# Optimization experiments

Measured on AMD Instinct MI355X. Metric: run time of the kernel, lower is better.

The kernel has to match this reference:

```python
import jax, jax.numpy as jnp
import numpy as np
from jax import lax


def setup_inputs() -> dict:
    key = jax.random.key(0)
    ks = jax.random.split(key, 20)
    B, D, T = 1024, 256, 128
    H, O = 256, 64
    f32 = jnp.float32
    rn = lambda k, shape, sc: jax.random.normal(k, shape, f32) * sc
    ru = lambda k, shape: jax.random.uniform(k, shape, f32)
    return {
        "x": jax.random.normal(ks[0], (B, D, T), f32),
        "W_in": rn(ks[1], (H, D), 1.0 / np.sqrt(D)),
        "b_in": rn(ks[2], (H,), 0.02),
        "beta1": ru(ks[3], (H,)),
        "thr1": ru(ks[4], (H,)),
        "W_h": rn(ks[5], (H, H), 1.0 / np.sqrt(H)),
        "b_h": rn(ks[6], (H,), 0.02),
        "beta2": ru(ks[7], (H,)),
        "thr2": ru(ks[8], (H,)),
        "W_h1": rn(ks[9], (H, H), 1.0 / np.sqrt(H)),
        "b_h1": rn(ks[10], (H,), 0.02),
        "W_f": rn(ks[11], (O, H), 1.0 / np.sqrt(H)),
        "b_f": rn(ks[12], (O,), 0.02),
        "beta_f": ru(ks[13], (O,)),
        "W_a": rn(ks[14], (O, H), 1.0 / np.sqrt(H)),
        "b_a": rn(ks[15], (O,), 0.02),
        "beta_a": ru(ks[16], (O,)),
    }


def _spike(u):
    # heaviside(u > 0); surrogate grad only matters in backward
    return (u > 0).astype(u.dtype)


def reference(x, W_in, b_in, beta1, thr1, W_h, b_h, beta2, thr2,
              W_h1, b_h1, W_f, b_f, beta_f, W_a, b_a, beta_a):
    B = x.shape[0]
    H0, H1, H2 = W_in.shape[0], W_h.shape[0], W_h1.shape[0]
    O = W_f.shape[0]
    dt = x.dtype
    # snntorch clamps learnable beta to [0, 1] in the state update
    b1c = jnp.clip(beta1, 0.0, 1.0)
    b2c = jnp.clip(beta2, 0.0, 1.0)
    bfc = jnp.clip(beta_f, 0.0, 1.0)
    bac = jnp.clip(beta_a, 0.0, 1.0)
    xT = jnp.transpose(x, (2, 0, 1))  # [T, B, D]

    def lif(mem, cur, bc, thr):
        # snntorch Leaky, reset_mechanism='subtract': reset from PREVIOUS mem (detached)
        reset = lax.stop_gradient(_spike(mem - thr))
        mem = bc * mem + cur - reset * thr
        spk = _spike(mem - thr)
        return spk, mem

    def step(carry, xt):
        m1, m2, m3, mf, ma = carry
        cur1 = xt @ W_in.T + b_in
        s1, m1 = lif(m1, cur1, b1c, thr1)
        cur2 = s1 @ W_h.T + b_h
        s2, m2 = lif(m2, cur2, b2c, thr2)
        # source bug preserved: third layer reuses lif_hidden (beta2, thr2)
        cur3 = s2 @ W_h1.T + b_h1
        s3, m3 = lif(m3, cur3, b2c, thr2)
        # output LI neurons: reset_mechanism='none'
        mf = bfc * mf + (s3 @ W_f.T + b_f)
        ma = bac * ma + (s3 @ W_a.T + b_a)
        return (m1, m2, m3, mf, ma), None

    z = lambda n: jnp.zeros((B, n), dt)
    init = (z(H0), z(H1), z(H2), z(O), z(O))
    (m1, m2, m3, mf, ma), _ = lax.scan(step, init, xT)
    return jax.nn.sigmoid(mf), jax.nn.sigmoid(ma)
```

## Files before the change

### kernel.cpp

```cpp
#include <hip/hip_runtime.h>
#include <math.h>
#include <stdint.h>


namespace {

constexpr int Bsz = 1024;
constexpr int Dd  = 256;
constexpr int Tt  = 128;
constexpr int Hh  = 256;
constexpr int Oo  = 64;

__global__ void pack_t(const float* __restrict__ W, float* __restrict__ Wt,
                       int R, int C) {
    int idx = blockIdx.x * 256 + threadIdx.x;
    if (idx >= (C + 1) * R) return;
    int c = idx / R, r = idx - c * R;
    Wt[idx] = (c < C) ? W[(size_t)r * C + c] : 0.f;
}

__global__ void pack_o(const float* __restrict__ Wf, const float* __restrict__ Wa,
                       float* __restrict__ WtO) {
    int idx = blockIdx.x * 256 + threadIdx.x;
    if (idx >= 257 * 128) return;
    int k = idx >> 7, o = idx & 127;
    float v = 0.f;
    if (k < 256) v = (o < 64) ? Wf[(size_t)o * 256 + k] : Wa[(size_t)(o - 64) * 256 + k];
    WtO[idx] = v;
}

__device__ __forceinline__ float clamp01(float v) { return fminf(fmaxf(v, 0.f), 1.f); }

__device__ __forceinline__ bool lif_step(float& m, float cur, float B, float Th) {
    const float r = (__fsub_rn(m, Th) > 0.f) ? Th : 0.f;
    m = __fsub_rn(__fadd_rn(__fmul_rn(B, m), cur), r);
    return __fsub_rn(m, Th) > 0.f;
}

__device__ __forceinline__ void make_masks(int nib, int lane, uint64_t* M) {
    #pragma unroll
    for (int q = 0; q < 4; ++q) {
        const int v   = __shfl(nib, 16 * q + (lane >> 2), 64);
        const int bit = (v >> (lane & 3)) & 1;
        M[q] = __ballot(bit != 0);
    }
}

__device__ __forceinline__ int compact(int nib, int lane, const uint64_t* M,
                                       uint16_t* lst) {
    const int p0 = (int)__popcll(M[0]);
    const int p1 = (int)__popcll(M[1]);
    const int p2 = (int)__popcll(M[2]);
    const int p3 = (int)__popcll(M[3]);
    const int q  = lane >> 4;
    const int base = ((q >= 1) ? p0 : 0) + ((q >= 2) ? p1 : 0) + ((q >= 3) ? p2 : 0);
    const uint64_t mq = (q & 2) ? ((q & 1) ? M[3] : M[2])
                                : ((q & 1) ? M[1] : M[0]);
    const int posb = (lane & 15) << 2;
    const int r0 = base + (int)__popcll(mq & ((1ull << posb) - 1ull));
    const int s1 = nib & 1;
    const int s2 = s1 + ((nib >> 1) & 1);
    const int s3 = s2 + ((nib >> 2) & 1);
    const int nb = lane << 2;
    if (nib & 1) lst[r0]      = (uint16_t)nb;
    if (nib & 2) lst[r0 + s1] = (uint16_t)(nb + 1);
    if (nib & 4) lst[r0 + s2] = (uint16_t)(nb + 2);
    if (nib & 8) lst[r0 + s3] = (uint16_t)(nb + 3);
    const int n    = p0 + p1 + p2 + p3;
    const int npad = (n + 7) & ~7;
    if (lane < npad - n) lst[n + lane] = (uint16_t)Hh;
    return npad;
}


__device__ __forceinline__ void issue8h(const char* __restrict__ tab,
                                        uint4 I, int offB, float4* w) {
    const int k[8] = {(int)(I.x & 0xffff), (int)(I.x >> 16),
                      (int)(I.y & 0xffff), (int)(I.y >> 16),
                      (int)(I.z & 0xffff), (int)(I.z >> 16),
                      (int)(I.w & 0xffff), (int)(I.w >> 16)};
    #pragma unroll
    for (int i = 0; i < 8; ++i)
        w[i] = *(const float4*)(tab + (k[i] << 10) + offB);
}

__device__ __forceinline__ void cons8h(float4& c, const float4* w) {
    #pragma unroll
    for (int i = 0; i < 8; ++i) {
        c.x = __fadd_rn(c.x, w[i].x);
        c.y = __fadd_rn(c.y, w[i].y);
        c.z = __fadd_rn(c.z, w[i].z);
        c.w = __fadd_rn(c.w, w[i].w);
    }
}

__device__ __forceinline__ float4 sum_h(const uint16_t* lst, int nbat,
                                        const float* __restrict__ tab, int offB) {
    float4 c = {0.f, 0.f, 0.f, 0.f};
    if (nbat == 0) return c;
    const char* tb = (const char*)tab;
    float4 A[8], B[8], C[8];
    issue8h(tb, *(const uint4*)(lst), offB, A);
    if (nbat == 1) { cons8h(c, A); return c; }
    issue8h(tb, *(const uint4*)(lst + 8), offB, B);
    if (nbat == 2) { cons8h(c, A); cons8h(c, B); return c; }
    issue8h(tb, *(const uint4*)(lst + 16), offB, C);
    __builtin_amdgcn_sched_barrier(0);
    int i = 3;
    for (; i + 2 < nbat; i += 3) {
        cons8h(c, A); issue8h(tb, *(const uint4*)(lst + 8 * i), offB, A);
        __builtin_amdgcn_sched_barrier(0);
        cons8h(c, B); issue8h(tb, *(const uint4*)(lst + 8 * (i + 1)), offB, B);
        __builtin_amdgcn_sched_barrier(0);
        cons8h(c, C); issue8h(tb, *(const uint4*)(lst + 8 * (i + 2)), offB, C);
        __builtin_amdgcn_sched_barrier(0);
    }
    const int r = nbat - i;
    if (r == 0) {
        cons8h(c, A); cons8h(c, B); cons8h(c, C);
    } else if (r == 1) {
        cons8h(c, A); issue8h(tb, *(const uint4*)(lst + 8 * i), offB, A);
        cons8h(c, B); cons8h(c, C); cons8h(c, A);
    } else {
        cons8h(c, A); issue8h(tb, *(const uint4*)(lst + 8 * i), offB, A);
        cons8h(c, B); issue8h(tb, *(const uint4*)(lst + 8 * (i + 1)), offB, B);
        cons8h(c, C); cons8h(c, A); cons8h(c, B);
    }
    return c;
}


__device__ __forceinline__ float2 sum_o_lds(const uint16_t* lst, int nbat,
                                            const float* tab, int offB) {
    float2 c = {0.f, 0.f};
    const char* tb = (const char*)tab;
    for (int i = 0; i < nbat; ++i) {
        const uint4 I = *(const uint4*)(lst + 8 * i);
        float2 w[8];
        w[0] = *(const float2*)(tb + ((I.x & 0xffffu) << 9) + offB);
        w[1] = *(const float2*)(tb + ((I.x >> 16)    << 9) + offB);
        w[2] = *(const float2*)(tb + ((I.y & 0xffffu) << 9) + offB);
        w[3] = *(const float2*)(tb + ((I.y >> 16)    << 9) + offB);
        w[4] = *(const float2*)(tb + ((I.z & 0xffffu) << 9) + offB);
        w[5] = *(const float2*)(tb + ((I.z >> 16)    << 9) + offB);
        w[6] = *(const float2*)(tb + ((I.w & 0xffffu) << 9) + offB);
        w[7] = *(const float2*)(tb + ((I.w >> 16)    << 9) + offB);
        #pragma unroll
        for (int j = 0; j < 8; ++j) {
            c.x = __fadd_rn(c.x, w[j].x);
            c.y = __fadd_rn(c.y, w[j].y);
        }
    }
    return c;
}

__global__ __launch_bounds__(256, 1) void snn_rec(
    const float* __restrict__ cur1,
    const float* __restrict__ Wt_h, const float* __restrict__ Wt_h1,
    const float* __restrict__ WtO,
    const float* __restrict__ beta1, const float* __restrict__ thr1,
    const float* __restrict__ b_h,  const float* __restrict__ beta2, const float* __restrict__ thr2,
    const float* __restrict__ b_h1,
    const float* __restrict__ b_f,  const float* __restrict__ beta_f,
    const float* __restrict__ b_a,  const float* __restrict__ beta_a,
    float* __restrict__ m1s, float* __restrict__ m2s, float* __restrict__ m3s,
    float* __restrict__ mos, float* __restrict__ out,
    int TC, int first)
{
    __shared__ __attribute__((aligned(16))) float ldsO[257 * 128];
    __shared__ __attribute__((aligned(16))) uint16_t lists[4][272];

    const int tid  = threadIdx.x;
    const int lane = tid & 63;
    const int b    = blockIdx.x * 4 + (tid >> 6);
    uint16_t* lst  = lists[tid >> 6];
    const int off4 = lane * 4;
    const int off2 = lane * 2;
    const int offBh = lane * 16;
    const int offBo = lane * 8;

    {
        const float4* s4 = (const float4*)WtO;
        float4* d4 = (float4*)ldsO;
        for (int v = tid; v < (257 * 128) / 4; v += 256) d4[v] = s4[v];
    }
    __syncthreads();

    const float4 B1v  = *(const float4*)(beta1 + off4);
    const float4 Th1v = *(const float4*)(thr1  + off4);
    const float4 bhv  = *(const float4*)(b_h   + off4);
    const float4 B2v  = *(const float4*)(beta2 + off4);
    const float4 Th2v = *(const float4*)(thr2  + off4);
    const float4 bh1v = *(const float4*)(b_h1  + off4);
    const float4 B1c  = {clamp01(B1v.x), clamp01(B1v.y), clamp01(B1v.z), clamp01(B1v.w)};
    const float4 B2c  = {clamp01(B2v.x), clamp01(B2v.y), clamp01(B2v.z), clamp01(B2v.w)};

    const int oo = off2 & 63;
    const float* bop = (lane < 32) ? b_f    : b_a;
    const float* Bop = (lane < 32) ? beta_f : beta_a;
    const float bo0 = bop[oo], bo1 = bop[oo + 1];
    const float Bo0 = clamp01(Bop[oo]), Bo1 = clamp01(Bop[oo + 1]);

    float4 m1, m2, m3;
    float mo0, mo1;
    if (first) {
        m1 = m2 = m3 = make_float4(0.f, 0.f, 0.f, 0.f);
        mo0 = mo1 = 0.f;
    } else {
        m1 = *(const float4*)(m1s + (size_t)b * Hh + off4);
        m2 = *(const float4*)(m2s + (size_t)b * Hh + off4);
        m3 = *(const float4*)(m3s + (size_t)b * Hh + off4);
        const float2 mo = *(const float2*)(mos + (size_t)b * 128 + off2);
        mo0 = mo.x; mo1 = mo.y;
    }

    const float* __restrict__ curb = cur1 + (size_t)b * TC * Hh + off4;
    float4 cur = *(const float4*)(curb);
    uint64_t M[4];

    for (int t = 0; t < TC; ++t) {
        int nib = 0;
        nib |= (int)lif_step(m1.x, cur.x, B1c.x, Th1v.x);
        nib |= (int)lif_step(m1.y, cur.y, B1c.y, Th1v.y) << 1;
        nib |= (int)lif_step(m1.z, cur.z, B1c.z, Th1v.z) << 2;
        nib |= (int)lif_step(m1.w, cur.w, B1c.w, Th1v.w) << 3;
        make_masks(nib, lane, M);
        int npad = compact(nib, lane, M, lst);
        if (t + 1 < TC) cur = *(const float4*)(curb + (size_t)(t + 1) * Hh);

        float4 s = sum_h(lst, npad >> 3, Wt_h, offBh);
        nib  = (int)lif_step(m2.x, __fadd_rn(s.x, bhv.x), B2c.x, Th2v.x);
        nib |= (int)lif_step(m2.y, __fadd_rn(s.y, bhv.y), B2c.y, Th2v.y) << 1;
        nib |= (int)lif_step(m2.z, __fadd_rn(s.z, bhv.z), B2c.z, Th2v.z) << 2;
        nib |= (int)lif_step(m2.w, __fadd_rn(s.w, bhv.w), B2c.w, Th2v.w) << 3;
        make_masks(nib, lane, M);
        npad = compact(nib, lane, M, lst);

        s = sum_h(lst, npad >> 3, Wt_h1, offBh);
        nib  = (int)lif_step(m3.x, __fadd_rn(s.x, bh1v.x), B2c.x, Th2v.x);
        nib |= (int)lif_step(m3.y, __fadd_rn(s.y, bh1v.y), B2c.y, Th2v.y) << 1;
        nib |= (int)lif_step(m3.z, __fadd_rn(s.z, bh1v.z), B2c.z, Th2v.z) << 2;
        nib |= (int)lif_step(m3.w, __fadd_rn(s.w, bh1v.w), B2c.w, Th2v.w) << 3;
        make_masks(nib, lane, M);
        npad = compact(nib, lane, M, lst);

        const float2 os = sum_o_lds(lst, npad >> 3, ldsO, offBo);
        mo0 = __fadd_rn(__fmul_rn(Bo0, mo0), __fadd_rn(os.x, bo0));
        mo1 = __fadd_rn(__fmul_rn(Bo1, mo1), __fadd_rn(os.y, bo1));
    }

    *(float4*)(m1s + (size_t)b * Hh + off4) = m1;
    *(float4*)(m2s + (size_t)b * Hh + off4) = m2;
    *(float4*)(m3s + (size_t)b * Hh + off4) = m3;
    *(float2*)(mos + (size_t)b * 128 + off2) = make_float2(mo0, mo1);

    float* dst = out + ((lane < 32) ? 0 : (size_t)Bsz * Oo) + (size_t)b * Oo + oo;
    const float o0 = (float)(1.0 / (1.0 + exp(-(double)mo0)));
    const float o1 = (float)(1.0 / (1.0 + exp(-(double)mo1)));
    *(float2*)dst = make_float2(o0, o1);
}

template<int TT>
__global__ __launch_bounds__(256) void gemm_l1_r8(
    const float* __restrict__ x, const float* __restrict__ Wt_in,
    const float* __restrict__ b_in, float* __restrict__ cur1,
    int tg_base, int TCloc)
{
    __shared__ float xs[Dd][TT];
    const int tid = threadIdx.x;
    const int b   = blockIdx.x;
    const int ty  = blockIdx.y;
    const int tg0 = tg_base + ty * TT;
    const float* xb = x + (size_t)b * Dd * Tt + tg0;
    constexpr int T4 = TT / 4;
    for (int v = tid; v < Dd * T4; v += 256) {
        const int d = v / T4, j4 = v - d * T4;
        *(float4*)&xs[d][j4 * 4] = *(const float4*)(xb + (size_t)d * Tt + j4 * 4);
    }
    __syncthreads();
    constexpr int TS = TT / 4;
    const int hq = tid & 63;
    const int tq = tid >> 6;
    float c0[TS], c1[TS], c2[TS], c3[TS];
    #pragma unroll
    for (int j = 0; j < TS; ++j) { c0[j] = 0.f; c1[j] = 0.f; c2[j] = 0.f; c3[j] = 0.f; }
    const float* wp = Wt_in + hq * 4;
    #pragma unroll 4
    for (int d = 0; d < Dd; ++d) {
        const float4 w = *(const float4*)(wp + (size_t)d * Hh);
        #pragma unroll
        for (int j = 0; j < TS; ++j) {
            const float xv = xs[d][tq * TS + j];
            c0[j] = fmaf(w.x, xv, c0[j]);
            c1[j] = fmaf(w.y, xv, c1[j]);
            c2[j] = fmaf(w.z, xv, c2[j]);
            c3[j] = fmaf(w.w, xv, c3[j]);
        }
    }
    const float4 bb = *(const float4*)(b_in + hq * 4);
    float* cb = cur1 + ((size_t)b * TCloc + ty * TT + tq * TS) * Hh + hq * 4;
    #pragma unroll
    for (int j = 0; j < TS; ++j) {
        float4 o;
        o.x = __fadd_rn(c0[j], bb.x);
        o.y = __fadd_rn(c1[j], bb.y);
        o.z = __fadd_rn(c2[j], bb.z);
        o.w = __fadd_rn(c3[j], bb.w);
        *(float4*)(cb + (size_t)j * Hh) = o;
    }
}

template<int TT>
__global__ __launch_bounds__(256) void gemm_l1_lds(
    const float* __restrict__ x, const float* __restrict__ Wt_in,
    const float* __restrict__ b_in, float* __restrict__ cur1,
    int tg_base, int TCloc)
{
    __shared__ float xs[Dd][TT];
    const int h   = threadIdx.x;
    const int b   = blockIdx.x;
    const int ty  = blockIdx.y;
    const int tg0 = tg_base + ty * TT;
    const float* xb = x + (size_t)b * Dd * Tt + tg0;
    constexpr int T4 = TT / 4;
    for (int v = threadIdx.x; v < Dd * T4; v += 256) {
        const int d = v / T4, j4 = v - d * T4;
        *(float4*)&xs[d][j4 * 4] = *(const float4*)(xb + (size_t)d * Tt + j4 * 4);
    }
    __syncthreads();
    float c[TT];
    #pragma unroll
    for (int j = 0; j < TT; ++j) c[j] = 0.f;
    for (int d = 0; d < Dd; ++d) {
        const float w = Wt_in[d * Hh + h];
        #pragma unroll
        for (int j = 0; j < TT; ++j) c[j] = fmaf(w, xs[d][j], c[j]);
    }
    const float bb = b_in[h];
    float* cb = cur1 + ((size_t)b * TCloc + ty * TT) * Hh;
    #pragma unroll
    for (int j = 0; j < TT; ++j) cb[j * Hh + h] = __fadd_rn(c[j], bb);
}

template<int TT>
__global__ __launch_bounds__(256) void gemm_l1_simple(
    const float* __restrict__ x, const float* __restrict__ Wt_in,
    const float* __restrict__ b_in, float* __restrict__ cur1, int tg0)
{
    const int h = threadIdx.x;
    const int b = blockIdx.x;
    float c[TT];
    #pragma unroll
    for (int j = 0; j < TT; ++j) c[j] = 0.f;
    const float* xb = x + (size_t)b * Dd * Tt + tg0;
    for (int d = 0; d < Dd; ++d) {
        const float w = Wt_in[d * Hh + h];
        const float* xp = xb + (size_t)d * Tt;
        #pragma unroll
        for (int j = 0; j < TT; ++j) c[j] = fmaf(w, xp[j], c[j]);
    }
    const float bb = b_in[h];
    float* cb = cur1 + (size_t)b * TT * Hh;
    #pragma unroll
    for (int j = 0; j < TT; ++j) cb[j * Hh + h] = __fadd_rn(c[j], bb);
}

}

extern "C" void kernel_launch(void* const* d_in, const int* in_sizes, int n_in,
                              void* d_out, int out_size, void* d_ws, size_t ws_size,
                              hipStream_t stream) {
    const float* x      = (const float*)d_in[0];
    const float* W_in   = (const float*)d_in[1];
    const float* b_in   = (const float*)d_in[2];
    const float* beta1  = (const float*)d_in[3];
    const float* thr1   = (const float*)d_in[4];
    const float* W_h    = (const float*)d_in[5];
    const float* b_h    = (const float*)d_in[6];
    const float* beta2  = (const float*)d_in[7];
    const float* thr2   = (const float*)d_in[8];
    const float* W_h1   = (const float*)d_in[9];
    const float* b_h1   = (const float*)d_in[10];
    const float* W_f    = (const float*)d_in[11];
    const float* b_f    = (const float*)d_in[12];
    const float* beta_f = (const float*)d_in[13];
    const float* W_a    = (const float*)d_in[14];
    const float* b_a    = (const float*)d_in[15];
    const float* beta_a = (const float*)d_in[16];
    float* out = (float*)d_out;

    float* ws = (float*)d_ws;
    size_t off = 0;
    auto alloc = [&](size_t n) { float* p = ws + off; off += n; return p; };
    float* Wt_in = alloc(257 * 256);
    float* Wt_h  = alloc(257 * 256);
    float* Wt_h1 = alloc(257 * 256);
    float* WtO   = alloc(257 * 128);
    float* m1s   = alloc((size_t)Bsz * Hh);
    float* m2s   = alloc((size_t)Bsz * Hh);
    float* m3s   = alloc((size_t)Bsz * Hh);
    float* mos   = alloc((size_t)Bsz * 128);
    const size_t fixed = off;

    int TC = 1;
    const int cands[8] = {128, 64, 32, 16, 8, 4, 2, 1};
    for (int i = 0; i < 8; ++i) {
        if ((fixed + (size_t)cands[i] * Bsz * Hh) * sizeof(float) <= ws_size) { TC = cands[i]; break; }
    }
    float* cur1 = alloc((size_t)TC * Bsz * Hh);

    pack_t<<<257, 256, 0, stream>>>(W_in, Wt_in, 256, 256);
    pack_t<<<257, 256, 0, stream>>>(W_h,  Wt_h,  256, 256);
    pack_t<<<257, 256, 0, stream>>>(W_h1, Wt_h1, 256, 256);
    pack_o<<<129, 256, 0, stream>>>(W_f, W_a, WtO);

    const int nch = Tt / TC;
    for (int c = 0; c < nch; ++c) {
        const int tg = c * TC;
        if (TC >= 32)
            gemm_l1_r8<32><<<dim3(Bsz, TC / 32), 256, 0, stream>>>(x, Wt_in, b_in, cur1, tg, TC);
        else if (TC == 16)
            gemm_l1_lds<16><<<dim3(Bsz, 1), 256, 0, stream>>>(x, Wt_in, b_in, cur1, tg, TC);
        else if (TC == 8)
            gemm_l1_lds<8><<<dim3(Bsz, 1), 256, 0, stream>>>(x, Wt_in, b_in, cur1, tg, TC);
        else if (TC == 4)
            gemm_l1_simple<4><<<Bsz, 256, 0, stream>>>(x, Wt_in, b_in, cur1, tg);
        else if (TC == 2)
            gemm_l1_simple<2><<<Bsz, 256, 0, stream>>>(x, Wt_in, b_in, cur1, tg);
        else
            gemm_l1_simple<1><<<Bsz, 256, 0, stream>>>(x, Wt_in, b_in, cur1, tg);

        snn_rec<<<Bsz / 4, 256, 0, stream>>>(
            cur1, Wt_h, Wt_h1, WtO,
            beta1, thr1, b_h, beta2, thr2, b_h1,
            b_f, beta_f, b_a, beta_a,
            m1s, m2s, m3s, mos, out, TC, (c == 0) ? 1 : 0);
    }
}
```

Measured before the change: 1.129 ms.

## Share one spike-union weight gather across four batch rows per block

Restructures the recurrent kernel so each wave owns 64 hidden units across the block's four batch rows, instead of each wave owning one batch row across all hidden units. Spike masks are published to shared memory with ballots, and the union of active inputs across the four rows is compacted into a list. Each list entry carries a 4-bit row mask, so one weight load feeds four accumulators. This cuts global weight gathers when rows share spikes, but adds three block-wide barriers per timestep and does wasted adds where the rows' spikes do not overlap. Separately, the input GEMM now prefetches the next weight row a loop iteration ahead.

Measured after the change: 2.483 ms. 2.2x slower.

```diff
diff --git a/kernel.cpp b/kernel.cpp
--- a/kernel.cpp
+++ b/kernel.cpp
@@ -37,17 +37,50 @@
     return __fsub_rn(m, Th) > 0.f;
 }
 
-__device__ __forceinline__ void make_masks(int nib, int lane, uint64_t* M) {
-    #pragma unroll
-    for (int q = 0; q < 4; ++q) {
-        const int v   = __shfl(nib, 16 * q + (lane >> 2), 64);
-        const int bit = (v >> (lane & 3)) & 1;
-        M[q] = __ballot(bit != 0);
-    }
-}
-
-__device__ __forceinline__ int compact(int nib, int lane, const uint64_t* M,
-                                       uint16_t* lst) {
+__device__ __forceinline__ int compact_u(int lane, const uint64_t (*mb)[4],
+                                         uint16_t* lst) {
+    const uint64_t m00 = mb[0][0], m10 = mb[1][0], m20 = mb[2][0], m30 = mb[3][0];
+    const uint64_t m01 = mb[0][1], m11 = mb[1][1], m21 = mb[2][1], m31 = mb[3][1];
+    const uint64_t m02 = mb[0][2], m12 = mb[1][2], m22 = mb[2][2], m32 = mb[3][2];
+    const uint64_t m03 = mb[0][3], m13 = mb[1][3], m23 = mb[2][3], m33 = mb[3][3];
+    const uint64_t U0 = m00 | m10 | m20 | m30;
+    const uint64_t U1 = m01 | m11 | m21 | m31;
+    const uint64_t U2 = m02 | m12 | m22 | m32;
+    const uint64_t U3 = m03 | m13 | m23 | m33;
+    const int p0 = (int)__popcll(U0);
+    const int p1 = (int)__popcll(U1);
+    const int p2 = (int)__popcll(U2);
+    const int p3 = (int)__popcll(U3);
+    const int q  = lane >> 4;
+    const uint64_t Uq = (q & 2) ? ((q & 1) ? U3 : U2) : ((q & 1) ? U1 : U0);
+    const uint64_t r0q = (q & 2) ? ((q & 1) ? m03 : m02) : ((q & 1) ? m01 : m00);
+    const uint64_t r1q = (q & 2) ? ((q & 1) ? m13 : m12) : ((q & 1) ? m11 : m10);
+    const uint64_t r2q = (q & 2) ? ((q & 1) ? m23 : m22) : ((q & 1) ? m21 : m20);
+    const uint64_t r3q = (q & 2) ? ((q & 1) ? m33 : m32) : ((q & 1) ? m31 : m30);
+    const int posb = (lane & 15) << 2;
+    const int nib  = (int)((Uq >> posb) & 0xFull);
+    const int base = ((q >= 1) ? p0 : 0) + ((q >= 2) ? p1 : 0) + ((q >= 3) ? p2 : 0);
+    const int r0   = base + (int)__popcll(Uq & ((1ull << posb) - 1ull));
+    const int s1 = nib & 1;
+    const int s2 = s1 + ((nib >> 1) & 1);
+    const int s3 = s2 + ((nib >> 2) & 1);
+    const int nb = lane << 2;
+    #define RM_AT(pos) ( (int)((r0q >> (pos)) & 1)        | ((int)((r1q >> (pos)) & 1) << 1) \
+                       | ((int)((r2q >> (pos)) & 1) << 2) | ((int)((r3q >> (pos)) & 1) << 3) )
+    if (nib & 1) lst[r0]      = (uint16_t)( nb      | (RM_AT(posb    ) << 12));
+    if (nib & 2) lst[r0 + s1] = (uint16_t)((nb + 1) | (RM_AT(posb + 1) << 12));
+    if (nib & 4) lst[r0 + s2] = (uint16_t)((nb + 2) | (RM_AT(posb + 2) << 12));
+    if (nib & 8) lst[r0 + s3] = (uint16_t)((nb + 3) | (RM_AT(posb + 3) << 12));
+    #undef RM_AT
+    const int n    = p0 + p1 + p2 + p3;
+    const int npad = (n + 7) & ~7;
+    if (lane < npad - n) lst[n + lane] = (uint16_t)Hh;
+    return npad;
+}
+
+__device__ __forceinline__ int compact_row(int lane, const uint64_t* M,
+                                           uint16_t* lst) {
+    const int nib = (int)((M[lane >> 4] >> ((lane & 15) << 2)) & 0xFull);
     const int p0 = (int)__popcll(M[0]);
     const int p1 = (int)__popcll(M[1]);
     const int p2 = (int)__popcll(M[2]);
@@ -73,60 +106,71 @@
 }
 
 
-__device__ __forceinline__ void issue8h(const char* __restrict__ tab,
-                                        uint4 I, int offB, float4* w) {
-    const int k[8] = {(int)(I.x & 0xffff), (int)(I.x >> 16),
-                      (int)(I.y & 0xffff), (int)(I.y >> 16),
-                      (int)(I.z & 0xffff), (int)(I.z >> 16),
-                      (int)(I.w & 0xffff), (int)(I.w >> 16)};
+__device__ __forceinline__ void issue8u(const char* __restrict__ tab,
+                                        uint4 I, int offW, float* w) {
+    const int k[8] = {(int)(I.x & 0xFFFu), (int)((I.x >> 16) & 0xFFFu),
+                      (int)(I.y & 0xFFFu), (int)((I.y >> 16) & 0xFFFu),
+                      (int)(I.z & 0xFFFu), (int)((I.z >> 16) & 0xFFFu),
+                      (int)(I.w & 0xFFFu), (int)((I.w >> 16) & 0xFFFu)};
     #pragma unroll
     for (int i = 0; i < 8; ++i)
-        w[i] = *(const float4*)(tab + (k[i] << 10) + offB);
-}
-
-__device__ __forceinline__ void cons8h(float4& c, const float4* w) {
+        w[i] = *(const float*)(tab + (k[i] << 10) + offW);
+}
+
+__device__ __forceinline__ void cons8u(float* acc, const float* w, uint4 I) {
+    const int rm[8] = {(int)((I.x >> 12) & 0xFu), (int)((I.x >> 28) & 0xFu),
+                       (int)((I.y >> 12) & 0xFu), (int)((I.y >> 28) & 0xFu),
+                       (int)((I.z >> 12) & 0xFu), (int)((I.z >> 28) & 0xFu),
+                       (int)((I.w >> 12) & 0xFu), (int)((I.w >> 28) & 0xFu)};
     #pragma unroll
     for (int i = 0; i < 8; ++i) {
-        c.x = __fadd_rn(c.x, w[i].x);
-        c.y = __fadd_rn(c.y, w[i].y);
-        c.z = __fadd_rn(c.z, w[i].z);
-        c.w = __fadd_rn(c.w, w[i].w);
-    }
-}
-
-__device__ __forceinline__ float4 sum_h(const uint16_t* lst, int nbat,
-                                        const float* __restrict__ tab, int offB) {
-    float4 c = {0.f, 0.f, 0.f, 0.f};
-    if (nbat == 0) return c;
+        acc[0] = __fadd_rn(acc[0], (rm[i] & 1) ? w[i] : 0.0f);
+        acc[1] = __fadd_rn(acc[1], (rm[i] & 2) ? w[i] : 0.0f);
+        acc[2] = __fadd_rn(acc[2], (rm[i] & 4) ? w[i] : 0.0f);
+        acc[3] = __fadd_rn(acc[3], (rm[i] & 8) ? w[i] : 0.0f);
+    }
+}
+
+__device__ __forceinline__ void sum_hu(const uint16_t* lst, int nbat,
+                                       const float* __restrict__ tab, int offW,
+                                       float* acc) {
+    acc[0] = 0.f; acc[1] = 0.f; acc[2] = 0.f; acc[3] = 0.f;
+    if (nbat == 0) return;
     const char* tb = (const char*)tab;
-    float4 A[8], B[8], C[8];
-    issue8h(tb, *(const uint4*)(lst), offB, A);
-    if (nbat == 1) { cons8h(c, A); return c; }
-    issue8h(tb, *(const uint4*)(lst + 8), offB, B);
-    if (nbat == 2) { cons8h(c, A); cons8h(c, B); return c; }
-    issue8h(tb, *(const uint4*)(lst + 16), offB, C);
+    uint4 IA, IB, IC;
+    float WA[8], WB[8], WC[8];
+    IA = *(const uint4*)(lst);      issue8u(tb, IA, offW, WA);
+    if (nbat == 1) { cons8u(acc, WA, IA); return; }
+    IB = *(const uint4*)(lst + 8);  issue8u(tb, IB, offW, WB);
+    if (nbat == 2) { cons8u(acc, WA, IA); cons8u(acc, WB, IB); return; }
+    IC = *(const uint4*)(lst + 16); issue8u(tb, IC, offW, WC);
     __builtin_amdgcn_sched_barrier(0);
     int i = 3;
     for (; i + 2 < nbat; i += 3) {
-        cons8h(c, A); issue8h(tb, *(const uint4*)(lst + 8 * i), offB, A);
+        cons8u(acc, WA, IA);
+        IA = *(const uint4*)(lst + 8 * i);       issue8u(tb, IA, offW, WA);
         __builtin_amdgcn_sched_barrier(0);
-        cons8h(c, B); issue8h(tb, *(const uint4*)(lst + 8 * (i + 1)), offB, B);
+        cons8u(acc, WB, IB);
+        IB = *(const uint4*)(lst + 8 * (i + 1)); issue8u(tb, IB, offW, WB);
         __builtin_amdgcn_sched_barrier(0);
-        cons8h(c, C); issue8h(tb, *(const uint4*)(lst + 8 * (i + 2)), offB, C);
+        cons8u(acc, WC, IC);
+        IC = *(const uint4*)(lst + 8 * (i + 2)); issue8u(tb, IC, offW, WC);
         __builtin_amdgcn_sched_barrier(0);
     }
     const int r = nbat - i;
     if (r == 0) {
-        cons8h(c, A); cons8h(c, B); cons8h(c, C);
+        cons8u(acc, WA, IA); cons8u(acc, WB, IB); cons8u(acc, WC, IC);
     } else if (r == 1) {
-        cons8h(c, A); issue8h(tb, *(const uint4*)(lst + 8 * i), offB, A);
-        cons8h(c, B); cons8h(c, C); cons8h(c, A);
+        cons8u(acc, WA, IA);
+        IA = *(const uint4*)(lst + 8 * i); issue8u(tb, IA, offW, WA);
+        cons8u(acc, WB, IB); cons8u(acc, WC, IC); cons8u(acc, WA, IA);
     } else {
-        cons8h(c, A); issue8h(tb, *(const uint4*)(lst + 8 * i), offB, A);
-        cons8h(c, B); issue8h(tb, *(const uint4*)(lst + 8 * (i + 1)), offB, B);
-        cons8h(c, C); cons8h(c, A); cons8h(c, B);
-    }
-    return c;
+        cons8u(acc, WA, IA);
+        IA = *(const uint4*)(lst + 8 * i);       issue8u(tb, IA, offW, WA);
+        cons8u(acc, WB, IB);
+        IB = *(const uint4*)(lst + 8 * (i + 1)); issue8u(tb, IB, offW, WB);
+        cons8u(acc, WC, IC); cons8u(acc, WA, IA); cons8u(acc, WB, IB);
+    }
 }
 
 
@@ -169,14 +213,17 @@
 {
     __shared__ __attribute__((aligned(16))) float ldsO[257 * 128];
     __shared__ __attribute__((aligned(16))) uint16_t lists[4][272];
+    __shared__ __attribute__((aligned(16))) uint64_t mbuf[2][3][4][4];
 
     const int tid  = threadIdx.x;
     const int lane = tid & 63;
-    const int b    = blockIdx.x * 4 + (tid >> 6);
-    uint16_t* lst  = lists[tid >> 6];
-    const int off4 = lane * 4;
+    const int wq   = tid >> 6;
+    const int b0   = blockIdx.x * 4;
+    const int brow = b0 + wq;
+    uint16_t* lst  = lists[wq];
+    const int hq   = wq * 64 + lane;
+    const int offW = hq * 4;
     const int off2 = lane * 2;
-    const int offBh = lane * 16;
     const int offBo = lane * 8;
 
     {
@@ -186,14 +233,12 @@
     }
     __syncthreads();
 
-    const float4 B1v  = *(const float4*)(beta1 + off4);
-    const float4 Th1v = *(const float4*)(thr1  + off4);
-    const float4 bhv  = *(const float4*)(b_h   + off4);
-    const float4 B2v  = *(const float4*)(beta2 + off4);
-    const float4 Th2v = *(const float4*)(thr2  + off4);
-    const float4 bh1v = *(const float4*)(b_h1  + off4);
-    const float4 B1c  = {clamp01(B1v.x), clamp01(B1v.y), clamp01(B1v.z), clamp01(B1v.w)};
-    const float4 B2c  = {clamp01(B2v.x), clamp01(B2v.y), clamp01(B2v.z), clamp01(B2v.w)};
+    const float B1s  = clamp01(beta1[hq]);
+    const float Th1s = thr1[hq];
+    const float bhs  = b_h[hq];
+    const float B2s  = clamp01(beta2[hq]);
+    const float Th2s = thr2[hq];
+    const float bh1s = b_h1[hq];
 
     const int oo = off2 & 63;
     const float* bop = (lane < 32) ? b_f    : b_a;
@@ -201,60 +246,91 @@
     const float bo0 = bop[oo], bo1 = bop[oo + 1];
     const float Bo0 = clamp01(Bop[oo]), Bo1 = clamp01(Bop[oo + 1]);
 
-    float4 m1, m2, m3;
+    float m1a[4], m2a[4], m3a[4];
     float mo0, mo1;
     if (first) {
-        m1 = m2 = m3 = make_float4(0.f, 0.f, 0.f, 0.f);
+        #pragma unroll
+        for (int r = 0; r < 4; ++r) { m1a[r] = 0.f; m2a[r] = 0.f; m3a[r] = 0.f; }
         mo0 = mo1 = 0.f;
     } else {
-        m1 = *(const float4*)(m1s + (size_t)b * Hh + off4);
-        m2 = *(const float4*)(m2s + (size_t)b * Hh + off4);
-        m3 = *(const float4*)(m3s + (size_t)b * Hh + off4);
-        const float2 mo = *(const float2*)(mos + (size_t)b * 128 + off2);
+        #pragma unroll
+        for (int r = 0; r < 4; ++r) {
+            m1a[r] = m1s[(size_t)(b0 + r) * Hh + hq];
+            m2a[r] = m2s[(size_t)(b0 + r) * Hh + hq];
+            m3a[r] = m3s[(size_t)(b0 + r) * Hh + hq];
+        }
+        const float2 mo = *(const float2*)(mos + (size_t)brow * 128 + off2);
         mo0 = mo.x; mo1 = mo.y;
     }
 
-    const float* __restrict__ curb = cur1 + (size_t)b * TC * Hh + off4;
-    float4 cur = *(const float4*)(curb);
-    uint64_t M[4];
+    const float* __restrict__ curb0 = cur1 + ((size_t)(b0 + 0) * TC) * Hh + hq;
+    const float* __restrict__ curb1 = cur1 + ((size_t)(b0 + 1) * TC) * Hh + hq;
+    const float* __restrict__ curb2 = cur1 + ((size_t)(b0 + 2) * TC) * Hh + hq;
+    const float* __restrict__ curb3 = cur1 + ((size_t)(b0 + 3) * TC) * Hh + hq;
+    float cur0 = curb0[0], cur1v = curb1[0], cur2v = curb2[0], cur3v = curb3[0];
+
+    float acc[4];
 
     for (int t = 0; t < TC; ++t) {
-        int nib = 0;
-        nib |= (int)lif_step(m1.x, cur.x, B1c.x, Th1v.x);
-        nib |= (int)lif_step(m1.y, cur.y, B1c.y, Th1v.y) << 1;
-        nib |= (int)lif_step(m1.z, cur.z, B1c.z, Th1v.z) << 2;
-        nib |= (int)lif_step(m1.w, cur.w, B1c.w, Th1v.w) << 3;
-        make_masks(nib, lane, M);
-        int npad = compact(nib, lane, M, lst);
-        if (t + 1 < TC) cur = *(const float4*)(curb + (size_t)(t + 1) * Hh);
-
-        float4 s = sum_h(lst, npad >> 3, Wt_h, offBh);
-        nib  = (int)lif_step(m2.x, __fadd_rn(s.x, bhv.x), B2c.x, Th2v.x);
-        nib |= (int)lif_step(m2.y, __fadd_rn(s.y, bhv.y), B2c.y, Th2v.y) << 1;
-        nib |= (int)lif_step(m2.z, __fadd_rn(s.z, bhv.z), B2c.z, Th2v.z) << 2;
-        nib |= (int)lif_step(m2.w, __fadd_rn(s.w, bhv.w), B2c.w, Th2v.w) << 3;
-        make_masks(nib, lane, M);
-        npad = compact(nib, lane, M, lst);
-
-        s = sum_h(lst, npad >> 3, Wt_h1, offBh);
-        nib  = (int)lif_step(m3.x, __fadd_rn(s.x, bh1v.x), B2c.x, Th2v.x);
-        nib |= (int)lif_step(m3.y, __fadd_rn(s.y, bh1v.y), B2c.y, Th2v.y) << 1;
-        nib |= (int)lif_step(m3.z, __fadd_rn(s.z, bh1v.z), B2c.z, Th2v.z) << 2;
-        nib |= (int)lif_step(m3.w, __fadd_rn(s.w, bh1v.w), B2c.w, Th2v.w) << 3;
-        make_masks(nib, lane, M);
-        npad = compact(nib, lane, M, lst);
-
-        const float2 os = sum_o_lds(lst, npad >> 3, ldsO, offBo);
+        const int par = t & 1;
+        const uint64_t W0 = __ballot(lif_step(m1a[0], cur0,  B1s, Th1s));
+        const uint64_t W1 = __ballot(lif_step(m1a[1], cur1v, B1s, Th1s));
+        const uint64_t W2 = __ballot(lif_step(m1a[2], cur2v, B1s, Th1s));
+        const uint64_t W3 = __ballot(lif_step(m1a[3], cur3v, B1s, Th1s));
+        if (lane == 0) {
+            mbuf[par][0][0][wq] = W0; mbuf[par][0][1][wq] = W1;
+            mbuf[par][0][2][wq] = W2; mbuf[par][0][3][wq] = W3;
+        }
+        if (t + 1 < TC) {
+            cur0  = curb0[(size_t)(t + 1) * Hh];
+            cur1v = curb1[(size_t)(t + 1) * Hh];
+            cur2v = curb2[(size_t)(t + 1) * Hh];
+            cur3v = curb3[(size_t)(t + 1) * Hh];
+        }
+        __syncthreads();
+
+        int npad = compact_u(lane, mbuf[par][0], lst);
+        sum_hu(lst, npad >> 3, Wt_h, offW, acc);
+        const uint64_t V0 = __ballot(lif_step(m2a[0], __fadd_rn(acc[0], bhs), B2s, Th2s));
+        const uint64_t V1 = __ballot(lif_step(m2a[1], __fadd_rn(acc[1], bhs), B2s, Th2s));
+        const uint64_t V2 = __ballot(lif_step(m2a[2], __fadd_rn(acc[2], bhs), B2s, Th2s));
+        const uint64_t V3 = __ballot(lif_step(m2a[3], __fadd_rn(acc[3], bhs), B2s, Th2s));
+        if (lane == 0) {
+            mbuf[par][1][0][wq] = V0; mbuf[par][1][1][wq] = V1;
+            mbuf[par][1][2][wq] = V2; mbuf[par][1][3][wq] = V3;
+        }
+        __syncthreads();
+
+        npad = compact_u(lane, mbuf[par][1], lst);
+        sum_hu(lst, npad >> 3, Wt_h1, offW, acc);
+        const uint64_t X0 = __ballot(lif_step(m3a[0], __fadd_rn(acc[0], bh1s), B2s, Th2s));
+        const uint64_t X1 = __ballot(lif_step(m3a[1], __fadd_rn(acc[1], bh1s), B2s, Th2s));
+        const uint64_t X2 = __ballot(lif_step(m3a[2], __fadd_rn(acc[2], bh1s), B2s, Th2s));
+        const uint64_t X3 = __ballot(lif_step(m3a[3], __fadd_rn(acc[3], bh1s), B2s, Th2s));
+        if (lane == 0) {
+            mbuf[par][2][0][wq] = X0; mbuf[par][2][1][wq] = X1;
+            mbuf[par][2][2][wq] = X2; mbuf[par][2][3][wq] = X3;
+        }
+        __syncthreads();
+
+        uint64_t M3r[4];
+        #pragma unroll
+        for (int q = 0; q < 4; ++q) M3r[q] = mbuf[par][2][wq][q];
+        const int npo = compact_row(lane, M3r, lst);
+        const float2 os = sum_o_lds(lst, npo >> 3, ldsO, offBo);
         mo0 = __fadd_rn(__fmul_rn(Bo0, mo0), __fadd_rn(os.x, bo0));
         mo1 = __fadd_rn(__fmul_rn(Bo1, mo1), __fadd_rn(os.y, bo1));
     }
 
-    *(float4*)(m1s + (size_t)b * Hh + off4) = m1;
-    *(float4*)(m2s + (size_t)b * Hh + off4) = m2;
-    *(float4*)(m3s + (size_t)b * Hh + off4) = m3;
-    *(float2*)(mos + (size_t)b * 128 + off2) = make_float2(mo0, mo1);
-
-    float* dst = out + ((lane < 32) ? 0 : (size_t)Bsz * Oo) + (size_t)b * Oo + oo;
+    #pragma unroll
+    for (int r = 0; r < 4; ++r) {
+        m1s[(size_t)(b0 + r) * Hh + hq] = m1a[r];
+        m2s[(size_t)(b0 + r) * Hh + hq] = m2a[r];
+        m3s[(size_t)(b0 + r) * Hh + hq] = m3a[r];
+    }
+    *(float2*)(mos + (size_t)brow * 128 + off2) = make_float2(mo0, mo1);
+
+    float* dst = out + ((lane < 32) ? 0 : (size_t)Bsz * Oo) + (size_t)brow * Oo + oo;
     const float o0 = (float)(1.0 / (1.0 + exp(-(double)mo0)));
     const float o1 = (float)(1.0 / (1.0 + exp(-(double)mo1)));
     *(float2*)dst = make_float2(o0, o1);
@@ -285,9 +361,11 @@
     #pragma unroll
     for (int j = 0; j < TS; ++j) { c0[j] = 0.f; c1[j] = 0.f; c2[j] = 0.f; c3[j] = 0.f; }
     const float* wp = Wt_in + hq * 4;
+    float4 w = *(const float4*)(wp);
     #pragma unroll 4
     for (int d = 0; d < Dd; ++d) {
-        const float4 w = *(const float4*)(wp + (size_t)d * Hh);
+        float4 wn;
+        if (d + 1 < Dd) wn = *(const float4*)(wp + (size_t)(d + 1) * Hh);
         #pragma unroll
         for (int j = 0; j < TS; ++j) {
             const float xv = xs[d][tq * TS + j];
@@ -296,6 +374,7 @@
             c2[j] = fmaf(w.z, xv, c2[j]);
             c3[j] = fmaf(w.w, xv, c3[j]);
         }
+        w = wn;
     }
     const float4 bb = *(const float4*)(b_in + hq * 4);
     float* cb = cur1 + ((size_t)b * TCloc + ty * TT + tq * TS) * Hh + hq * 4;
```
